# Kernel tuning notes

Measured on AMD Instinct MI355X. Metric: run time of the kernel, lower is better.

Reference implementation:

```python
import jax, jax.numpy as jnp
import numpy as np
from math import pi as PI, log

B, N, D, K = 16, 16384, 64, 64


def setup_inputs() -> dict:
    key = jax.random.key(0)
    k1, k2, k3, k4 = jax.random.split(key, 4)
    x = jax.random.normal(k1, (B, N, D), dtype=jnp.float32)
    pi_w = jax.nn.softmax(jax.random.normal(k2, (K,), dtype=jnp.float32))  # mixture weights, sum to 1
    mu = jax.random.normal(k3, (K, D), dtype=jnp.float32)
    var = jax.random.uniform(k4, (K, D), dtype=jnp.float32, minval=0.5, maxval=1.5)  # diagonal variances
    return {"x": x, "pi": pi_w, "mu": mu, "var": var}


def reference(x, pi, mu, var):
    b, n, d = x.shape
    # --- gmm.predict_proba: diagonal-covariance Gaussian log-likelihoods + log pi, softmax over K ---
    inv_var = 1.0 / var                                   # (K, D)
    x2 = x * x                                            # (B, N, D)
    # Mahalanobis distance expanded via matmuls to avoid a (B,N,K,D) intermediate
    maha = (jnp.einsum('bnd,kd->bnk', x2, inv_var)
            - 2.0 * jnp.einsum('bnd,kd->bnk', x, mu * inv_var)
            + jnp.sum(mu * mu * inv_var, axis=-1))        # (B, N, K)
    log_det = jnp.sum(jnp.log(var), axis=-1)              # (K,)
    log_prob = -0.5 * (d * log(2.0 * PI) + log_det + maha)
    Q = jax.nn.softmax(log_prob + jnp.log(pi), axis=-1)   # (B, N, K) responsibilities
    # --- weighted reductions over N ---
    Q_sum = jnp.sum(Q, axis=1) / n                         # (B, K)
    Q_x = jnp.einsum('bnk,bnd->bkd', Q, x) / n             # (B, K, D)
    Q_x2 = jnp.einsum('bnk,bnd->bkd', Q, x2) / n           # (B, K, D)
    # --- Fisher-vector statistics ---
    d_pi = Q_sum - pi                                      # (B, K)
    qs = Q_sum[..., None]                                  # (B, K, 1)
    d_mu = Q_x - qs * mu
    d_sigma = -Q_x2 - qs * (mu * mu) + qs * var + 2.0 * Q_x * mu
    return jnp.concatenate([d_pi.reshape(b, -1), d_mu.reshape(b, -1), d_sigma.reshape(b, -1)], axis=1)
```

## Files before the change

kernel.cpp:

```cpp
#include <hip/hip_runtime.h>
#include <hip/hip_bf16.h>
#include <math.h>

#define B_  16
#define N_  16384
#define D_  64
#define K_  64
#define OUT_PER_B (K_ + 2*K_*D_)
#define CHUNKS 64
#define NTILES (N_ / CHUNKS / 64)

#define PART_STRIDE (64*4 + 2*4096*2)
#define PART_TOTAL  ((size_t)B_ * CHUNKS * PART_STRIDE)
#define W_OFF   PART_TOTAL
#define C0_OFF  (PART_TOTAL + 16384)

typedef float f32x4 __attribute__((ext_vector_type(4)));
typedef short short8 __attribute__((ext_vector_type(8)));

union U8 { short8 s8; unsigned int u[4]; };

__device__ __forceinline__ unsigned short f2bf(float f) {
    union { float f; unsigned int u; } v; v.f = f;
    unsigned int r = v.u + 0x7FFFu + ((v.u >> 16) & 1u);
    return (unsigned short)(r >> 16);
}

__device__ __forceinline__ unsigned int f2bf2(float lo, float hi) {
    __hip_bfloat162 h = __float22bfloat162_rn(make_float2(lo, hi));
    unsigned int u;
    __builtin_memcpy(&u, &h, 4);
    return u;
}

__device__ __forceinline__ float bf2f(unsigned short u) {
    unsigned int v = ((unsigned int)u) << 16;
    float f;
    __builtin_memcpy(&f, &v, 4);
    return f;
}

__global__ __launch_bounds__(256) void fv_prep(const float* __restrict__ pi,
                                               const float* __restrict__ mu,
                                               const float* __restrict__ var,
                                               char* __restrict__ ws) {
    __shared__ float red[256];
    const int t = threadIdx.x;

    {
        int k = t >> 2, pr = t & 3;
        float s = 0.0f;
        #pragma unroll
        for (int j = 0; j < 16; ++j) {
            int d = pr * 16 + j;
            float v = var[k * 64 + d];
            float m = mu[k * 64 + d];
            s += __logf(v) + m * m / v;
        }
        red[t] = s;
    }

    {
        const int lane = t & 63;
        const int kt   = t >> 6;
        const int r16  = lane & 15;
        const int q    = lane >> 4;
        const int k = 16 * kt + r16;
        const float* vr = var + k * 64 + 8 * q;
        const float* mr = mu  + k * 64 + 8 * q;
        float vv[16], mm[16];
        *(float4*)&vv[0]  = *(const float4*)(vr);
        *(float4*)&vv[4]  = *(const float4*)(vr + 4);
        *(float4*)&vv[8]  = *(const float4*)(vr + 32);
        *(float4*)&vv[12] = *(const float4*)(vr + 36);
        *(float4*)&mm[0]  = *(const float4*)(mr);
        *(float4*)&mm[4]  = *(const float4*)(mr + 4);
        *(float4*)&mm[8]  = *(const float4*)(mr + 32);
        *(float4*)&mm[12] = *(const float4*)(mr + 36);
        float iv[16];
        #pragma unroll
        for (int i = 0; i < 16; ++i) iv[i] = 1.0f / vv[i];
        U8 h0, h1, h2, h3;
        #pragma unroll
        for (int i = 0; i < 4; ++i) {
            h0.u[i] = f2bf2(-0.5f * iv[2*i],     -0.5f * iv[2*i + 1]);
            h1.u[i] = f2bf2(-0.5f * iv[8 + 2*i], -0.5f * iv[8 + 2*i + 1]);
            h2.u[i] = f2bf2(mm[2*i] * iv[2*i],   mm[2*i+1] * iv[2*i + 1]);
            h3.u[i] = f2bf2(mm[8+2*i] * iv[8+2*i], mm[8+2*i+1] * iv[8+2*i+1]);
        }
        short8* W = (short8*)(ws + W_OFF);
        W[(kt * 4 + 0) * 64 + lane] = h0.s8;
        W[(kt * 4 + 1) * 64 + lane] = h1.s8;
        W[(kt * 4 + 2) * 64 + lane] = h2.s8;
        W[(kt * 4 + 3) * 64 + lane] = h3.s8;
    }

    __syncthreads();
    if ((t & 3) == 0) {
        int k = t >> 2;
        float sum = red[4 * k] + red[4 * k + 1] + red[4 * k + 2] + red[4 * k + 3];
        ((float*)(ws + C0_OFF))[k] = __logf(pi[k]) - 0.5f * (117.6241322502f + sum);
    }
}

__global__ __launch_bounds__(256, 4) void fv_main(const float* __restrict__ x,
                                                  char* __restrict__ partials) {
    __shared__ __align__(16) unsigned short QtS[2][64 * 72];
    __shared__ __align__(16) unsigned short wfS[4 * 4 * 64 * 8];
    __shared__ float qsum_s[4][64];

    const int t    = threadIdx.x;
    const int w    = t >> 6;
    const int lane = t & 63;
    const int r16  = lane & 15;
    const int q    = lane >> 4;

    {
        const float4* gw = (const float4*)(partials + W_OFF);
        float4* sw = (float4*)wfS;
        #pragma unroll
        for (int i = 0; i < 4; ++i) sw[i * 256 + t] = gw[i * 256 + t];
    }
    f32x4 c0v[4];
    {
        const float* c0g = (const float*)(partials + C0_OFF);
        #pragma unroll
        for (int kt = 0; kt < 4; ++kt)
            c0v[kt] = *(const f32x4*)&c0g[16 * kt + 4 * q];
    }

    const int bi    = blockIdx.y;
    const int chunk = blockIdx.x;
    const int ppb   = N_ / CHUNKS;
    const float* xb = x + ((size_t)bi * N_ + (size_t)chunk * ppb) * D_;

    f32x4 accX[4]  = {};
    f32x4 accX2[4] = {};
    float qsacc[4][4] = {};

    const int rowoff = (16 * w + r16) * D_ + 8 * q;
    const int dcol   = 16 * w + r16;

    const short8* wfp = (const short8*)wfS;

    __syncthreads();

    #pragma unroll 1
    for (int tile = 0; tile < NTILES; ++tile) {
        const float* xt = xb + (size_t)tile * 64 * D_;

        float4 va, vb, vc, vd;
        {
            const float* xr = xt + rowoff;
            va = *(const float4*)(xr);
            vb = *(const float4*)(xr + 4);
            vc = *(const float4*)(xr + 32);
            vd = *(const float4*)(xr + 36);
        }

        U8 fxa, fxb, fx2a, fx2b;
        fxa.u[0]  = f2bf2(va.x, va.y);           fxa.u[1]  = f2bf2(va.z, va.w);
        fxa.u[2]  = f2bf2(vb.x, vb.y);           fxa.u[3]  = f2bf2(vb.z, vb.w);
        fxb.u[0]  = f2bf2(vc.x, vc.y);           fxb.u[1]  = f2bf2(vc.z, vc.w);
        fxb.u[2]  = f2bf2(vd.x, vd.y);           fxb.u[3]  = f2bf2(vd.z, vd.w);
        fx2a.u[0] = f2bf2(va.x*va.x, va.y*va.y); fx2a.u[1] = f2bf2(va.z*va.z, va.w*va.w);
        fx2a.u[2] = f2bf2(vb.x*vb.x, vb.y*vb.y); fx2a.u[3] = f2bf2(vb.z*vb.z, vb.w*vb.w);
        fx2b.u[0] = f2bf2(vc.x*vc.x, vc.y*vc.y); fx2b.u[1] = f2bf2(vc.z*vc.z, vc.w*vc.w);
        fx2b.u[2] = f2bf2(vd.x*vd.x, vd.y*vd.y); fx2b.u[3] = f2bf2(vd.z*vd.z, vd.w*vd.w);

        float sc[4][4];
        #pragma unroll
        for (int kt = 0; kt < 4; ++kt) {
            f32x4 a = c0v[kt];
            a = __builtin_amdgcn_mfma_f32_16x16x32_bf16(wfp[(kt*4+0)*64 + lane], fx2a.s8, a, 0, 0, 0);
            a = __builtin_amdgcn_mfma_f32_16x16x32_bf16(wfp[(kt*4+1)*64 + lane], fx2b.s8, a, 0, 0, 0);
            a = __builtin_amdgcn_mfma_f32_16x16x32_bf16(wfp[(kt*4+2)*64 + lane], fxa.s8,  a, 0, 0, 0);
            a = __builtin_amdgcn_mfma_f32_16x16x32_bf16(wfp[(kt*4+3)*64 + lane], fxb.s8,  a, 0, 0, 0);
            sc[kt][0] = a[0]; sc[kt][1] = a[1]; sc[kt][2] = a[2]; sc[kt][3] = a[3];
        }

        float mx = sc[0][0];
        #pragma unroll
        for (int kt = 0; kt < 4; ++kt)
            #pragma unroll
            for (int rr = 0; rr < 4; ++rr) mx = fmaxf(mx, sc[kt][rr]);
        mx = fmaxf(mx, __shfl_xor(mx, 16));
        mx = fmaxf(mx, __shfl_xor(mx, 32));
        float z = 0.0f;
        #pragma unroll
        for (int kt = 0; kt < 4; ++kt)
            #pragma unroll
            for (int rr = 0; rr < 4; ++rr) {
                sc[kt][rr] = __expf(sc[kt][rr] - mx);
                z += sc[kt][rr];
            }
        z += __shfl_xor(z, 16);
        z += __shfl_xor(z, 32);
        float inv = 1.0f / z;

        float vle[16];
        {
            const float* xc = xt + dcol;
            #pragma unroll
            for (int c = 0; c < 2; ++c)
                #pragma unroll
                for (int j = 0; j < 8; ++j)
                    vle[8 * c + j] = xc[(32 * c + 8 * q + j) * D_];
        }

        const int p = 16 * w + r16;
        unsigned short* Qb = QtS[tile & 1];
        #pragma unroll
        for (int kt = 0; kt < 4; ++kt) {
            #pragma unroll
            for (int rr = 0; rr < 4; rr += 2) {
                float q0 = sc[kt][rr] * inv;
                float q1 = sc[kt][rr + 1] * inv;
                qsacc[kt][rr]     += q0;
                qsacc[kt][rr + 1] += q1;
                unsigned int pk = f2bf2(q0, q1);
                Qb[(16 * kt + 4 * q + rr)     * 72 + p] = (unsigned short)pk;
                Qb[(16 * kt + 4 * q + rr + 1) * 72 + p] = (unsigned short)(pk >> 16);
            }
        }

        asm volatile("s_waitcnt lgkmcnt(0)\n\ts_barrier" ::: "memory");

        U8 fxp0, fxp1, fx2p0, fx2p1;
        #pragma unroll
        for (int i = 0; i < 4; ++i) {
            float a0 = vle[2 * i], a1 = vle[2 * i + 1];
            float b0 = vle[8 + 2 * i], b1 = vle[8 + 2 * i + 1];
            fxp0.u[i]  = f2bf2(a0, a1);
            fxp1.u[i]  = f2bf2(b0, b1);
            fx2p0.u[i] = f2bf2(a0 * a0, a1 * a1);
            fx2p1.u[i] = f2bf2(b0 * b0, b1 * b1);
        }
        #pragma unroll
        for (int kt = 0; kt < 4; ++kt) {
            const unsigned short* qr = &Qb[(16 * kt + r16) * 72 + 8 * q];
            short8 aq0 = *(const short8*)(const void*)(qr);
            short8 aq1 = *(const short8*)(const void*)(qr + 32);
            accX[kt]  = __builtin_amdgcn_mfma_f32_16x16x32_bf16(aq0, fxp0.s8,  accX[kt],  0, 0, 0);
            accX2[kt] = __builtin_amdgcn_mfma_f32_16x16x32_bf16(aq0, fx2p0.s8, accX2[kt], 0, 0, 0);
            accX[kt]  = __builtin_amdgcn_mfma_f32_16x16x32_bf16(aq1, fxp1.s8,  accX[kt],  0, 0, 0);
            accX2[kt] = __builtin_amdgcn_mfma_f32_16x16x32_bf16(aq1, fx2p1.s8, accX2[kt], 0, 0, 0);
        }
    }

    char* rec = partials + ((size_t)bi * CHUNKS + chunk) * PART_STRIDE;
    float* part_qs = (float*)rec;
    unsigned short* part_qx  = (unsigned short*)(rec + 256);
    unsigned short* part_qx2 = part_qx + 4096;
    #pragma unroll
    for (int kt = 0; kt < 4; ++kt)
        #pragma unroll
        for (int rr = 0; rr < 4; ++rr) {
            int k = 16 * kt + 4 * q + rr;
            part_qx [k * 64 + 16 * w + r16] = f2bf(accX[kt][rr]);
            part_qx2[k * 64 + 16 * w + r16] = f2bf(accX2[kt][rr]);
        }
    #pragma unroll
    for (int kt = 0; kt < 4; ++kt)
        #pragma unroll
        for (int rr = 0; rr < 4; ++rr) {
            float v = qsacc[kt][rr];
            v += __shfl_xor(v, 1);
            v += __shfl_xor(v, 2);
            v += __shfl_xor(v, 4);
            v += __shfl_xor(v, 8);
            if (r16 == 0) qsum_s[w][16 * kt + 4 * q + rr] = v;
        }
    __syncthreads();
    if (t < 64)
        part_qs[t] = qsum_s[0][t] + qsum_s[1][t] + qsum_s[2][t] + qsum_s[3][t];
}

__global__ __launch_bounds__(256) void fv_finalize(const float* __restrict__ pi,
                                                   const float* __restrict__ mu,
                                                   const float* __restrict__ var,
                                                   const char* __restrict__ partials,
                                                   float* __restrict__ out) {
    const int bk   = blockIdx.x;
    const int b    = bk >> 6;
    const int k    = bk & 63;
    const int t    = threadIdx.x;
    const int cg   = t >> 6;
    const int lane = t & 63;
    const int cs   = lane >> 3;
    const int dg   = lane & 7;

    const char* base = partials + (size_t)b * CHUNKS * PART_STRIDE;

    float qx[8]  = {};
    float qx2[8] = {};
    float qs = 0.0f;
    #pragma unroll
    for (int i = 0; i < 2; ++i) {
        const char* r = base + (size_t)(16 * cg + 8 * i + cs) * PART_STRIDE;
        short8 vx  = *(const short8*)(const void*)(r + 256 + k * 128 + dg * 16);
        short8 vx2 = *(const short8*)(const void*)(r + 256 + 8192 + k * 128 + dg * 16);
        if (dg == 0) qs += ((const float*)r)[k];
        #pragma unroll
        for (int j = 0; j < 8; ++j) {
            qx[j]  += bf2f((unsigned short)vx[j]);
            qx2[j] += bf2f((unsigned short)vx2[j]);
        }
    }

    #pragma unroll
    for (int m = 8; m <= 32; m <<= 1) {
        #pragma unroll
        for (int j = 0; j < 8; ++j) {
            qx[j]  += __shfl_xor(qx[j],  m);
            qx2[j] += __shfl_xor(qx2[j], m);
        }
    }
    qs += __shfl_xor(qs, 1);
    qs += __shfl_xor(qs, 2);
    qs += __shfl_xor(qs, 4);
    qs += __shfl_xor(qs, 8);
    qs += __shfl_xor(qs, 16);
    qs += __shfl_xor(qs, 32);

    __shared__ float sQx[4][64];
    __shared__ float sQx2[4][64];
    __shared__ float sQs[4];
    if (cs == 0) {
        #pragma unroll
        for (int j = 0; j < 8; ++j) {
            sQx[cg][dg * 8 + j]  = qx[j];
            sQx2[cg][dg * 8 + j] = qx2[j];
        }
    }
    if (lane == 0) sQs[cg] = qs;
    __syncthreads();

    if (cg == 0) {
        const int d = lane;
        const float invN = 1.0f / (float)N_;
        float QX  = sQx[0][d]  + sQx[1][d]  + sQx[2][d]  + sQx[3][d];
        float QX2 = sQx2[0][d] + sQx2[1][d] + sQx2[2][d] + sQx2[3][d];
        float QS  = sQs[0] + sQs[1] + sQs[2] + sQs[3];
        float m = mu[k * 64 + d];
        float v = var[k * 64 + d];
        float* ob = out + (size_t)b * OUT_PER_B;
        if (d == 0) ob[k] = QS * invN - pi[k];
        ob[64 + k * 64 + d]        = (QX - QS * m) * invN;
        ob[64 + 4096 + k * 64 + d] = (-QX2 - QS * m * m + QS * v + 2.0f * QX * m) * invN;
    }
}

extern "C" void kernel_launch(void* const* d_in, const int* in_sizes, int n_in,
                              void* d_out, int out_size, void* d_ws, size_t ws_size,
                              hipStream_t stream) {
    const float* x   = (const float*)d_in[0];
    const float* pi  = (const float*)d_in[1];
    const float* mu  = (const float*)d_in[2];
    const float* var = (const float*)d_in[3];
    char* ws = (char*)d_ws;

    fv_prep<<<1, 256, 0, stream>>>(pi, mu, var, ws);
    fv_main<<<dim3(CHUNKS, B_), 256, 0, stream>>>(x, ws);
    fv_finalize<<<B_ * K_, 256, 0, stream>>>(pi, mu, var, ws, (float*)d_out);
}
```

Baseline: 120.7 us.

## Fuse prep, main and finalize into one cooperative kernel with grid sync

Merges the three kernels into a single cooperative launch. Each block recomputes the GMM weight fragments and constants into shared memory, runs the main responsibility/accumulation loop, then a grid-wide sync replaces the kernel boundary before the same blocks do the finalize reduction. The aim is to remove two launch gaps and the serial single-block prep kernel. In exchange every block redundantly recomputes the prep work, and the grid barrier needs all 1024 blocks co-resident, which depends on the occupancy check (4 blocks per CU).

Result: no change. 119.9 us (-0.7%).

```diff
diff --git a/kernel.cpp b/kernel.cpp
--- a/kernel.cpp
+++ b/kernel.cpp
@@ -1,6 +1,9 @@
 #include <hip/hip_runtime.h>
+#include <hip/hip_cooperative_groups.h>
 #include <hip/hip_bf16.h>
 #include <math.h>
+
+namespace cg = cooperative_groups;
 
 #define B_  16
 #define N_  16384
@@ -40,13 +43,303 @@
     return f;
 }
 
+__global__ __launch_bounds__(256, 4) void fv_fused(const float* __restrict__ x,
+                                                   const float* __restrict__ pi,
+                                                   const float* __restrict__ mu,
+                                                   const float* __restrict__ var,
+                                                   char* __restrict__ partials,
+                                                   float* __restrict__ out) {
+    __shared__ __align__(16) unsigned short QtS[2][64 * 72];
+    __shared__ __align__(16) unsigned short wfS[4 * 4 * 64 * 8];
+    __shared__ float qsum_s[4][64];
+    __shared__ float red[256];
+    __shared__ __align__(16) float c0s[64];
+
+    const int t    = threadIdx.x;
+    const int w    = t >> 6;
+    const int lane = t & 63;
+    const int r16  = lane & 15;
+    const int q    = lane >> 4;
+
+    {
+        int k = t >> 2, pr = t & 3;
+        float s = 0.0f;
+        #pragma unroll
+        for (int j = 0; j < 16; ++j) {
+            int d = pr * 16 + j;
+            float v = var[k * 64 + d];
+            float m = mu[k * 64 + d];
+            s += __logf(v) + m * m / v;
+        }
+        red[t] = s;
+    }
+    {
+        const int kt = t >> 6;
+        const int k = 16 * kt + r16;
+        const float* vr = var + k * 64 + 8 * q;
+        const float* mr = mu  + k * 64 + 8 * q;
+        float vv[16], mm[16];
+        *(float4*)&vv[0]  = *(const float4*)(vr);
+        *(float4*)&vv[4]  = *(const float4*)(vr + 4);
+        *(float4*)&vv[8]  = *(const float4*)(vr + 32);
+        *(float4*)&vv[12] = *(const float4*)(vr + 36);
+        *(float4*)&mm[0]  = *(const float4*)(mr);
+        *(float4*)&mm[4]  = *(const float4*)(mr + 4);
+        *(float4*)&mm[8]  = *(const float4*)(mr + 32);
+        *(float4*)&mm[12] = *(const float4*)(mr + 36);
+        float iv[16];
+        #pragma unroll
+        for (int i = 0; i < 16; ++i) iv[i] = 1.0f / vv[i];
+        U8 h0, h1, h2, h3;
+        #pragma unroll
+        for (int i = 0; i < 4; ++i) {
+            h0.u[i] = f2bf2(-0.5f * iv[2*i],     -0.5f * iv[2*i + 1]);
+            h1.u[i] = f2bf2(-0.5f * iv[8 + 2*i], -0.5f * iv[8 + 2*i + 1]);
+            h2.u[i] = f2bf2(mm[2*i] * iv[2*i],   mm[2*i+1] * iv[2*i + 1]);
+            h3.u[i] = f2bf2(mm[8+2*i] * iv[8+2*i], mm[8+2*i+1] * iv[8+2*i+1]);
+        }
+        short8* W = (short8*)wfS;
+        W[(kt * 4 + 0) * 64 + lane] = h0.s8;
+        W[(kt * 4 + 1) * 64 + lane] = h1.s8;
+        W[(kt * 4 + 2) * 64 + lane] = h2.s8;
+        W[(kt * 4 + 3) * 64 + lane] = h3.s8;
+    }
+    __syncthreads();
+    if ((t & 3) == 0) {
+        int k = t >> 2;
+        float sum = red[4 * k] + red[4 * k + 1] + red[4 * k + 2] + red[4 * k + 3];
+        c0s[k] = __logf(pi[k]) - 0.5f * (117.6241322502f + sum);
+    }
+    __syncthreads();
+
+    f32x4 c0v[4];
+    #pragma unroll
+    for (int kt = 0; kt < 4; ++kt)
+        c0v[kt] = *(const f32x4*)&c0s[16 * kt + 4 * q];
+
+    const int bi    = blockIdx.y;
+    const int chunk = blockIdx.x;
+    const int ppb   = N_ / CHUNKS;
+    const float* xb = x + ((size_t)bi * N_ + (size_t)chunk * ppb) * D_;
+
+    f32x4 accX[4]  = {};
+    f32x4 accX2[4] = {};
+    float qsacc[4][4] = {};
+
+    const int rowoff = (16 * w + r16) * D_ + 8 * q;
+    const int dcol   = 16 * w + r16;
+
+    const short8* wfp = (const short8*)wfS;
+
+    #pragma unroll 1
+    for (int tile = 0; tile < NTILES; ++tile) {
+        const float* xt = xb + (size_t)tile * 64 * D_;
+
+        float4 va, vb, vc, vd;
+        {
+            const float* xr = xt + rowoff;
+            va = *(const float4*)(xr);
+            vb = *(const float4*)(xr + 4);
+            vc = *(const float4*)(xr + 32);
+            vd = *(const float4*)(xr + 36);
+        }
+
+        U8 fxa, fxb, fx2a, fx2b;
+        fxa.u[0]  = f2bf2(va.x, va.y);           fxa.u[1]  = f2bf2(va.z, va.w);
+        fxa.u[2]  = f2bf2(vb.x, vb.y);           fxa.u[3]  = f2bf2(vb.z, vb.w);
+        fxb.u[0]  = f2bf2(vc.x, vc.y);           fxb.u[1]  = f2bf2(vc.z, vc.w);
+        fxb.u[2]  = f2bf2(vd.x, vd.y);           fxb.u[3]  = f2bf2(vd.z, vd.w);
+        fx2a.u[0] = f2bf2(va.x*va.x, va.y*va.y); fx2a.u[1] = f2bf2(va.z*va.z, va.w*va.w);
+        fx2a.u[2] = f2bf2(vb.x*vb.x, vb.y*vb.y); fx2a.u[3] = f2bf2(vb.z*vb.z, vb.w*vb.w);
+        fx2b.u[0] = f2bf2(vc.x*vc.x, vc.y*vc.y); fx2b.u[1] = f2bf2(vc.z*vc.z, vc.w*vc.w);
+        fx2b.u[2] = f2bf2(vd.x*vd.x, vd.y*vd.y); fx2b.u[3] = f2bf2(vd.z*vd.z, vd.w*vd.w);
+
+        float sc[4][4];
+        #pragma unroll
+        for (int kt = 0; kt < 4; ++kt) {
+            f32x4 a = c0v[kt];
+            a = __builtin_amdgcn_mfma_f32_16x16x32_bf16(wfp[(kt*4+0)*64 + lane], fx2a.s8, a, 0, 0, 0);
+            a = __builtin_amdgcn_mfma_f32_16x16x32_bf16(wfp[(kt*4+1)*64 + lane], fx2b.s8, a, 0, 0, 0);
+            a = __builtin_amdgcn_mfma_f32_16x16x32_bf16(wfp[(kt*4+2)*64 + lane], fxa.s8,  a, 0, 0, 0);
+            a = __builtin_amdgcn_mfma_f32_16x16x32_bf16(wfp[(kt*4+3)*64 + lane], fxb.s8,  a, 0, 0, 0);
+            sc[kt][0] = a[0]; sc[kt][1] = a[1]; sc[kt][2] = a[2]; sc[kt][3] = a[3];
+        }
+
+        float mx = sc[0][0];
+        #pragma unroll
+        for (int kt = 0; kt < 4; ++kt)
+            #pragma unroll
+            for (int rr = 0; rr < 4; ++rr) mx = fmaxf(mx, sc[kt][rr]);
+        mx = fmaxf(mx, __shfl_xor(mx, 16));
+        mx = fmaxf(mx, __shfl_xor(mx, 32));
+        float z = 0.0f;
+        #pragma unroll
+        for (int kt = 0; kt < 4; ++kt)
+            #pragma unroll
+            for (int rr = 0; rr < 4; ++rr) {
+                sc[kt][rr] = __expf(sc[kt][rr] - mx);
+                z += sc[kt][rr];
+            }
+        z += __shfl_xor(z, 16);
+        z += __shfl_xor(z, 32);
+        float inv = 1.0f / z;
+
+        float vle[16];
+        {
+            const float* xc = xt + dcol;
+            #pragma unroll
+            for (int c = 0; c < 2; ++c)
+                #pragma unroll
+                for (int j = 0; j < 8; ++j)
+                    vle[8 * c + j] = xc[(32 * c + 8 * q + j) * D_];
+        }
+
+        const int p = 16 * w + r16;
+        unsigned short* Qb = QtS[tile & 1];
+        #pragma unroll
+        for (int kt = 0; kt < 4; ++kt) {
+            #pragma unroll
+            for (int rr = 0; rr < 4; rr += 2) {
+                float q0 = sc[kt][rr] * inv;
+                float q1 = sc[kt][rr + 1] * inv;
+                qsacc[kt][rr]     += q0;
+                qsacc[kt][rr + 1] += q1;
+                unsigned int pk = f2bf2(q0, q1);
+                Qb[(16 * kt + 4 * q + rr)     * 72 + p] = (unsigned short)pk;
+                Qb[(16 * kt + 4 * q + rr + 1) * 72 + p] = (unsigned short)(pk >> 16);
+            }
+        }
+
+        asm volatile("s_waitcnt lgkmcnt(0)\n\ts_barrier" ::: "memory");
+
+        U8 fxp0, fxp1, fx2p0, fx2p1;
+        #pragma unroll
+        for (int i = 0; i < 4; ++i) {
+            float a0 = vle[2 * i], a1 = vle[2 * i + 1];
+            float b0 = vle[8 + 2 * i], b1 = vle[8 + 2 * i + 1];
+            fxp0.u[i]  = f2bf2(a0, a1);
+            fxp1.u[i]  = f2bf2(b0, b1);
+            fx2p0.u[i] = f2bf2(a0 * a0, a1 * a1);
+            fx2p1.u[i] = f2bf2(b0 * b0, b1 * b1);
+        }
+        #pragma unroll
+        for (int kt = 0; kt < 4; ++kt) {
+            const unsigned short* qr = &Qb[(16 * kt + r16) * 72 + 8 * q];
+            short8 aq0 = *(const short8*)(const void*)(qr);
+            short8 aq1 = *(const short8*)(const void*)(qr + 32);
+            accX[kt]  = __builtin_amdgcn_mfma_f32_16x16x32_bf16(aq0, fxp0.s8,  accX[kt],  0, 0, 0);
+            accX2[kt] = __builtin_amdgcn_mfma_f32_16x16x32_bf16(aq0, fx2p0.s8, accX2[kt], 0, 0, 0);
+            accX[kt]  = __builtin_amdgcn_mfma_f32_16x16x32_bf16(aq1, fxp1.s8,  accX[kt],  0, 0, 0);
+            accX2[kt] = __builtin_amdgcn_mfma_f32_16x16x32_bf16(aq1, fx2p1.s8, accX2[kt], 0, 0, 0);
+        }
+    }
+
+    char* rec = partials + ((size_t)bi * CHUNKS + chunk) * PART_STRIDE;
+    float* part_qs = (float*)rec;
+    unsigned short* part_qx  = (unsigned short*)(rec + 256);
+    unsigned short* part_qx2 = part_qx + 4096;
+    #pragma unroll
+    for (int kt = 0; kt < 4; ++kt)
+        #pragma unroll
+        for (int rr = 0; rr < 4; ++rr) {
+            int k = 16 * kt + 4 * q + rr;
+            part_qx [k * 64 + 16 * w + r16] = f2bf(accX[kt][rr]);
+            part_qx2[k * 64 + 16 * w + r16] = f2bf(accX2[kt][rr]);
+        }
+    #pragma unroll
+    for (int kt = 0; kt < 4; ++kt)
+        #pragma unroll
+        for (int rr = 0; rr < 4; ++rr) {
+            float v = qsacc[kt][rr];
+            v += __shfl_xor(v, 1);
+            v += __shfl_xor(v, 2);
+            v += __shfl_xor(v, 4);
+            v += __shfl_xor(v, 8);
+            if (r16 == 0) qsum_s[w][16 * kt + 4 * q + rr] = v;
+        }
+    __syncthreads();
+    if (t < 64)
+        part_qs[t] = qsum_s[0][t] + qsum_s[1][t] + qsum_s[2][t] + qsum_s[3][t];
+
+    __threadfence();
+    cg::this_grid().sync();
+    __threadfence();
+
+    {
+        const int b    = blockIdx.y;
+        const int k    = blockIdx.x;
+        const int cgp  = t >> 6;
+        const int cs   = lane >> 3;
+        const int dg   = lane & 7;
+
+        const char* base = partials + (size_t)b * CHUNKS * PART_STRIDE;
+
+        float qx[8]  = {};
+        float qx2[8] = {};
+        float qs = 0.0f;
+        #pragma unroll
+        for (int i = 0; i < 2; ++i) {
+            const char* r = base + (size_t)(16 * cgp + 8 * i + cs) * PART_STRIDE;
+            short8 vx  = *(const short8*)(const void*)(r + 256 + k * 128 + dg * 16);
+            short8 vx2 = *(const short8*)(const void*)(r + 256 + 8192 + k * 128 + dg * 16);
+            if (dg == 0) qs += ((const float*)r)[k];
+            #pragma unroll
+            for (int j = 0; j < 8; ++j) {
+                qx[j]  += bf2f((unsigned short)vx[j]);
+                qx2[j] += bf2f((unsigned short)vx2[j]);
+            }
+        }
+
+        #pragma unroll
+        for (int m = 8; m <= 32; m <<= 1) {
+            #pragma unroll
+            for (int j = 0; j < 8; ++j) {
+                qx[j]  += __shfl_xor(qx[j],  m);
+                qx2[j] += __shfl_xor(qx2[j], m);
+            }
+        }
+        qs += __shfl_xor(qs, 1);
+        qs += __shfl_xor(qs, 2);
+        qs += __shfl_xor(qs, 4);
+        qs += __shfl_xor(qs, 8);
+        qs += __shfl_xor(qs, 16);
+        qs += __shfl_xor(qs, 32);
+
+        float (*sQx)[64]  = qsum_s;
+        float (*sQx2)[64] = (float (*)[64])red;
+        float* sQs = c0s;
+        if (cs == 0) {
+            #pragma unroll
+            for (int j = 0; j < 8; ++j) {
+                sQx[cgp][dg * 8 + j]  = qx[j];
+                sQx2[cgp][dg * 8 + j] = qx2[j];
+            }
+        }
+        if (lane == 0) sQs[cgp] = qs;
+        __syncthreads();
+
+        if (cgp == 0) {
+            const int d = lane;
+            const float invN = 1.0f / (float)N_;
+            float QX  = sQx[0][d]  + sQx[1][d]  + sQx[2][d]  + sQx[3][d];
+            float QX2 = sQx2[0][d] + sQx2[1][d] + sQx2[2][d] + sQx2[3][d];
+            float QS  = sQs[0] + sQs[1] + sQs[2] + sQs[3];
+            float m = mu[k * 64 + d];
+            float v = var[k * 64 + d];
+            float* ob = out + (size_t)b * OUT_PER_B;
+            if (d == 0) ob[k] = QS * invN - pi[k];
+            ob[64 + k * 64 + d]        = (QX - QS * m) * invN;
+            ob[64 + 4096 + k * 64 + d] = (-QX2 - QS * m * m + QS * v + 2.0f * QX * m) * invN;
+        }
+    }
+}
+
 __global__ __launch_bounds__(256) void fv_prep(const float* __restrict__ pi,
                                                const float* __restrict__ mu,
                                                const float* __restrict__ var,
                                                char* __restrict__ ws) {
     __shared__ float red[256];
     const int t = threadIdx.x;
-
     {
         int k = t >> 2, pr = t & 3;
         float s = 0.0f;
@@ -59,7 +352,6 @@
         }
         red[t] = s;
     }
-
     {
         const int lane = t & 63;
         const int kt   = t >> 6;
@@ -94,7 +386,6 @@
         W[(kt * 4 + 2) * 64 + lane] = h2.s8;
         W[(kt * 4 + 3) * 64 + lane] = h3.s8;
     }
-
     __syncthreads();
     if ((t & 3) == 0) {
         int k = t >> 2;
@@ -148,7 +439,6 @@
     #pragma unroll 1
     for (int tile = 0; tile < NTILES; ++tile) {
         const float* xt = xb + (size_t)tile * 64 * D_;
-
         float4 va, vb, vc, vd;
         {
             const float* xr = xt + rowoff;
@@ -157,7 +447,6 @@
             vc = *(const float4*)(xr + 32);
             vd = *(const float4*)(xr + 36);
         }
-
         U8 fxa, fxb, fx2a, fx2b;
         fxa.u[0]  = f2bf2(va.x, va.y);           fxa.u[1]  = f2bf2(va.z, va.w);
         fxa.u[2]  = f2bf2(vb.x, vb.y);           fxa.u[3]  = f2bf2(vb.z, vb.w);
@@ -285,7 +574,7 @@
     const int b    = bk >> 6;
     const int k    = bk & 63;
     const int t    = threadIdx.x;
-    const int cg   = t >> 6;
+    const int cgp  = t >> 6;
     const int lane = t & 63;
     const int cs   = lane >> 3;
     const int dg   = lane & 7;
@@ -297,7 +586,7 @@
     float qs = 0.0f;
     #pragma unroll
     for (int i = 0; i < 2; ++i) {
-        const char* r = base + (size_t)(16 * cg + 8 * i + cs) * PART_STRIDE;
+        const char* r = base + (size_t)(16 * cgp + 8 * i + cs) * PART_STRIDE;
         short8 vx  = *(const short8*)(const void*)(r + 256 + k * 128 + dg * 16);
         short8 vx2 = *(const short8*)(const void*)(r + 256 + 8192 + k * 128 + dg * 16);
         if (dg == 0) qs += ((const float*)r)[k];
@@ -307,7 +596,6 @@
             qx2[j] += bf2f((unsigned short)vx2[j]);
         }
     }
-
     #pragma unroll
     for (int m = 8; m <= 32; m <<= 1) {
         #pragma unroll
@@ -329,14 +617,14 @@
     if (cs == 0) {
         #pragma unroll
         for (int j = 0; j < 8; ++j) {
-            sQx[cg][dg * 8 + j]  = qx[j];
-            sQx2[cg][dg * 8 + j] = qx2[j];
-        }
-    }
-    if (lane == 0) sQs[cg] = qs;
+            sQx[cgp][dg * 8 + j]  = qx[j];
+            sQx2[cgp][dg * 8 + j] = qx2[j];
+        }
+    }
+    if (lane == 0) sQs[cgp] = qs;
     __syncthreads();
 
-    if (cg == 0) {
+    if (cgp == 0) {
         const int d = lane;
         const float invN = 1.0f / (float)N_;
         float QX  = sQx[0][d]  + sQx[1][d]  + sQx[2][d]  + sQx[3][d];
@@ -359,8 +647,26 @@
     const float* mu  = (const float*)d_in[2];
     const float* var = (const float*)d_in[3];
     char* ws = (char*)d_ws;
+    float* outp = (float*)d_out;
+
+    static int use_coop = -1;
+    if (use_coop < 0) {
+        int maxb = 0;
+        hipError_t e = hipOccupancyMaxActiveBlocksPerMultiprocessor(
+            &maxb, (const void*)fv_fused, 256, 0);
+        use_coop = (e == hipSuccess && maxb >= 4) ? 1 : 0;
+    }
+
+    if (use_coop) {
+        void* args[] = {(void*)&x, (void*)&pi, (void*)&mu, (void*)&var,
+                        (void*)&ws, (void*)&outp};
+        hipError_t e = hipLaunchCooperativeKernel(
+            (const void*)fv_fused, dim3(CHUNKS, B_), dim3(256), args, 0, stream);
+        if (e == hipSuccess) return;
+        use_coop = 0;
+    }
 
     fv_prep<<<1, 256, 0, stream>>>(pi, mu, var, ws);
     fv_main<<<dim3(CHUNKS, B_), 256, 0, stream>>>(x, ws);
-    fv_finalize<<<B_ * K_, 256, 0, stream>>>(pi, mu, var, ws, (float*)d_out);
-}
+    fv_finalize<<<B_ * K_, 256, 0, stream>>>(pi, mu, var, ws, outp);
+}
```
